# Optimization experiments

Measured on AMD Instinct MI355X. Metric: run time of the kernel, lower is better.

The kernel has to match this reference:

```python
import jax, jax.numpy as jnp
import numpy as np

B, IN_CH, HID, OUT_CH, GH, GW = 16, 64, 128, 64, 64, 64


def grid_edges(h, w):
    # torch_geometric.utils.grid: 8-neighborhood + self-loop, edge = (node, node+offset)
    idx = np.arange(h * w).reshape(h, w)
    rows, cols = [], []
    for dr in (-1, 0, 1):
        for dc in (-1, 0, 1):
            node = idx[max(0, -dr):h - max(0, dr), max(0, -dc):w - max(0, dc)]
            nb = idx[max(0, dr):h + min(0, dr) or None, max(0, dc):w + min(0, dc) or None]
            rows.append(node.ravel())
            cols.append(nb.ravel())
    return np.stack([np.concatenate(rows), np.concatenate(cols)])


def setup_inputs() -> dict:
    key = jax.random.key(0)
    ks = jax.random.split(key, 32)
    def rn(i, shape, scale=0.05):
        return jax.random.normal(ks[i], shape, dtype=jnp.float32) * scale
    e = grid_edges(GH, GW)                                   # (2, E)
    offs = (np.arange(B) * (GH * GW)).reshape(B, 1, 1)
    ei = (e[None] + offs).transpose(1, 0, 2).reshape(2, -1)  # (2, B*E) batched offsets
    return {
        "x": rn(0, (B, IN_CH, GH, GW), 1.0),
        "cW1": rn(1, (HID, IN_CH, 3, 3)), "cb1": rn(2, (HID,)),
        "cW2": rn(3, (IN_CH, HID, 3, 3)), "cb2": rn(4, (IN_CH,)),
        "q1W": rn(5, (HID, IN_CH)), "q1b": rn(6, (HID,)),
        "k1W": rn(7, (HID, IN_CH)), "k1b": rn(8, (HID,)),
        "v1W": rn(9, (HID, IN_CH)), "v1b": rn(10, (HID,)),
        "s1W": rn(11, (HID, IN_CH)), "s1b": rn(12, (HID,)),
        "q2W": rn(13, (IN_CH, HID)), "q2b": rn(14, (IN_CH,)),
        "k2W": rn(15, (IN_CH, HID)), "k2b": rn(16, (IN_CH,)),
        "v2W": rn(17, (IN_CH, HID)), "v2b": rn(18, (IN_CH,)),
        "s2W": rn(19, (IN_CH, HID)), "s2b": rn(20, (IN_CH,)),
        "fW1": rn(21, (HID, 2 * IN_CH, 3, 3)), "fb1": rn(22, (HID,)),
        "fW2": rn(23, (OUT_CH, HID, 3, 3)), "fb2": rn(24, (OUT_CH,)),
        "edge_index": jnp.asarray(ei, dtype=jnp.int32),
    }


def gelu(x):
    return jax.nn.gelu(x, approximate=False)


def sn_conv(x, W, b):
    # spectral_norm: power iteration on (O, I*k*k) matrix; u,v detached, grad through sigma
    O = W.shape[0]
    Wm = W.reshape(O, -1)
    u = jnp.ones((O,), W.dtype) / jnp.sqrt(jnp.asarray(O, W.dtype))
    for _ in range(3):
        v = Wm.T @ u
        v = v / (jnp.linalg.norm(v) + 1e-12)
        u = Wm @ v
        u = u / (jnp.linalg.norm(u) + 1e-12)
    u = jax.lax.stop_gradient(u)
    v = jax.lax.stop_gradient(v)
    sigma = u @ (Wm @ v)
    Wn = W / sigma
    xp = jnp.pad(x, ((0, 0), (0, 0), (1, 1), (1, 1)), mode='edge')  # replicate padding
    y = jax.lax.conv_general_dilated(xp, Wn, (1, 1), 'VALID',
                                     dimension_numbers=('NCHW', 'OIHW', 'NCHW'))
    return y + b[None, :, None, None]


def tconv(x, src, dst, N, heads, qW, qb, kW, kb, vW, vb, sW, sb):
    # PyG TransformerConv (concat=True, root_weight=True, no edge features)
    d = qW.shape[0] // heads
    q = (x @ qW.T + qb)[dst].reshape(-1, heads, d)
    k = (x @ kW.T + kb)[src].reshape(-1, heads, d)
    v = (x @ vW.T + vb)[src].reshape(-1, heads, d)
    alpha = (q * k).sum(-1) / jnp.sqrt(jnp.asarray(d, x.dtype))      # (E, heads)
    m = jax.ops.segment_max(alpha, dst, num_segments=N)               # scatter-softmax
    a = jnp.exp(alpha - m[dst])
    s = jax.ops.segment_sum(a, dst, num_segments=N)
    a = a / (s[dst] + 1e-16)
    out = jax.ops.segment_sum(a[:, :, None] * v, dst, num_segments=N)  # (N, heads, d)
    return out.reshape(N, heads * d) + x @ sW.T + sb


def reference(x, cW1, cb1, cW2, cb2, q1W, q1b, k1W, k1b, v1W, v1b, s1W, s1b,
              q2W, q2b, k2W, k2b, v2W, v2b, s2W, s2b, fW1, fb1, fW2, fb2, edge_index):
    Bb, C, Hc, Wc = x.shape
    N = Bb * Hc * Wc
    # CNN branch (DoubleConvBlock)
    x1 = gelu(sn_conv(gelu(sn_conv(x, cW1, cb1)), cW2, cb2))
    # GCN branch
    xf = x.transpose(0, 2, 3, 1).reshape(N, C)
    src, dst = edge_index[0], edge_index[1]
    h = gelu(tconv(xf, src, dst, N, 8, q1W, q1b, k1W, k1b, v1W, v1b, s1W, s1b))
    h = gelu(tconv(h, src, dst, N, 1, q2W, q2b, k2W, k2b, v2W, v2b, s2W, s2b))
    x2 = h.reshape(Bb, Hc, Wc, -1).transpose(0, 3, 1, 2)
    # Fusion
    xc = jnp.concatenate([x1, x2], axis=1)
    return gelu(sn_conv(gelu(sn_conv(xc, fW1, fb1)), fW2, fb2))
```

## Files before the change

### kernel.cpp

```cpp
#include <hip/hip_runtime.h>
#include <hip/hip_bf16.h>

typedef unsigned int  u32;
typedef unsigned short u16;
typedef __attribute__((ext_vector_type(8))) short bf16x8;
typedef __attribute__((ext_vector_type(4))) float f32x4;
typedef __attribute__((ext_vector_type(4))) u32 u32x4;

#define NPIX 65536

constexpr size_t SIG   = 0;
constexpr size_t B1OFF = 256;
constexpr size_t B2OFF = B1OFF + 2048;
constexpr size_t WC1   = B2OFF + 1024;
constexpr size_t WC2   = WC1 + 147456;
constexpr size_t WF1   = WC2 + 147456;
constexpr size_t WF2   = WF1 + 294912;
constexpr size_t WP1   = WF2 + 147456;
constexpr size_t WP2   = WP1 + 65536;
constexpr size_t XB    = WP2 + 65536;
constexpr size_t HBUF  = XB + 8388608;
constexpr size_t QKVS2 = HBUF + 16777216;
constexpr size_t XC    = QKVS2 + 33554432;
constexpr size_t QKVS1 = XC + 16777216;
constexpr size_t TBUF  = QKVS1 + 16777216;
constexpr size_t GRAM  = QKVS1 + 67108864;

__device__ __forceinline__ float gelu_f(float v) {
    float xa = fabsf(v) * 0.70710678118654752f;
    float t  = __fdividef(1.0f, fmaf(0.3275911f, xa, 1.0f));
    float poly = t * fmaf(t, fmaf(t, fmaf(t, fmaf(t, 1.061405429f, -1.453152027f),
                   1.421413741f), -0.284496736f), 0.254829592f);
    float erfv = 1.0f - poly * __expf(-xa * xa);
    erfv = copysignf(erfv, v);
    return 0.5f * v * (1.0f + erfv);
}
__device__ __forceinline__ u16 f2bf(float f) {
    __hip_bfloat16 b = __float2bfloat16(f);
    return *reinterpret_cast<u16*>(&b);
}
__device__ __forceinline__ float blo(u32 u) {
    union { u32 i; float f; } x; x.i = u << 16; return x.f;
}
__device__ __forceinline__ float bhi(u32 u) {
    union { u32 i; float f; } x; x.i = u & 0xffff0000u; return x.f;
}
__device__ __forceinline__ u32 packbf(float a, float b) {
    return (u32)f2bf(a) | ((u32)f2bf(b) << 16);
}
__device__ __forceinline__ void g2l16(const void* g, void* l) {
    __builtin_amdgcn_global_load_lds(
        (const __attribute__((address_space(1))) u32*)g,
        (__attribute__((address_space(3))) u32*)l, 16, 0, 0);
}

__device__ float block_sum(float vv, float* red) {
    #pragma unroll
    for (int m = 1; m < 64; m <<= 1) vv += __shfl_xor(vv, m);
    int tid = threadIdx.x;
    __syncthreads();
    if ((tid & 63) == 0) red[tid >> 6] = vv;
    __syncthreads();
    return red[0] + red[1] + red[2] + red[3];
}


__device__ void gram_body(int bid, char* smem,
                          const float* cW1, const float* cW2,
                          const float* fW1, const float* fW2, float* Gall) {
    const float* W; int O, K, wsel, tile;
    if (bid < 64)       { W = cW1; O = 128; K = 576;  wsel = 0; tile = bid; }
    else if (bid < 80)  { W = cW2; O = 64;  K = 1152; wsel = 1; tile = bid - 64; }
    else if (bid < 144) { W = fW1; O = 128; K = 1152; wsel = 2; tile = bid - 80; }
    else                { W = fW2; O = 64;  K = 1152; wsel = 3; tile = bid - 144; }
    int ntiles = O >> 4;
    int ti0 = (tile / ntiles) << 4, tj0 = (tile % ntiles) << 4;
    float (*Wi)[33] = (float(*)[33])smem;
    float (*Wj)[33] = (float(*)[33])(smem + 16 * 33 * 4);
    int tid = threadIdx.x;
    int ti = tid >> 4, tj = tid & 15;
    int r = tid >> 5, c = tid & 31;
    float acc = 0.f;
    for (int k0 = 0; k0 < K; k0 += 32) {
        Wi[r][c]     = W[(size_t)(ti0 + r) * K + k0 + c];
        Wi[r + 8][c] = W[(size_t)(ti0 + r + 8) * K + k0 + c];
        Wj[r][c]     = W[(size_t)(tj0 + r) * K + k0 + c];
        Wj[r + 8][c] = W[(size_t)(tj0 + r + 8) * K + k0 + c];
        __syncthreads();
        #pragma unroll
        for (int k = 0; k < 32; ++k)
            acc += Wi[ti][k] * Wj[tj][k];
        __syncthreads();
    }
    Gall[wsel * 16384 + (ti0 + ti) * 128 + (tj0 + tj)] = acc;
}

__device__ void convert_body(int bid, char* smem,
                             const float* __restrict__ x, u16* __restrict__ xb) {
    float (*tile)[65] = (float(*)[65])smem;
    int b = bid >> 6, y = bid & 63;
    int tid = threadIdx.x;
    #pragma unroll
    for (int i = 0; i < 16; ++i) {
        int c = (tid >> 6) + i * 4;
        tile[c][tid & 63] = x[(((size_t)b * 64 + c) << 12) + (y << 6) + (tid & 63)];
    }
    __syncthreads();
    #pragma unroll
    for (int i = 0; i < 16; ++i) {
        int idx = tid + i * 256;
        int p = idx >> 6, c = idx & 63;
        xb[(((size_t)b << 12) + (y << 6) + p) * 64 + c] = f2bf(tile[c][p]);
    }
}

__device__ void prep_proj_body(int bid,
               const float* q1W, const float* k1W, const float* v1W, const float* s1W,
               const float* q2W, const float* k2W, const float* v2W, const float* s2W,
               const float* q1b, const float* k1b, const float* v1b, const float* s1b,
               const float* q2b, const float* k2b, const float* v2b, const float* s2b,
               u16* wp1, u16* wp2, float* b1, float* b2) {
    const float* W1[4] = {q1W, k1W, v1W, s1W};
    const float* W2[4] = {q2W, k2W, v2W, s2W};
    const float* Bb1[4] = {q1b, k1b, v1b, s1b};
    const float* Bb2[4] = {q2b, k2b, v2b, s2b};
    int idx = bid * 256 + threadIdx.x;
    if (idx < 32768) {
        int w = idx >> 13, r = idx & 8191;
        wp1[(size_t)w * 8192 + r] = f2bf(W1[w][r]);
    } else if (idx < 65536) {
        int j = idx - 32768; int w = j >> 13, r = j & 8191;
        wp2[(size_t)w * 8192 + r] = f2bf(W2[w][r]);
    } else if (idx < 66048) {
        int j = idx - 65536; int w = j >> 7; b1[j] = Bb1[w][j & 127];
    } else if (idx < 66304) {
        int j = idx - 66048; int w = j >> 6; b2[j] = Bb2[w][j & 63];
    }
}

__device__ void prep_conv_w_body(int bx, int wsel,
                 const float* __restrict__ cW1, const float* __restrict__ cW2,
                 const float* __restrict__ fW1, const float* __restrict__ fW2,
                 const float* __restrict__ sig,
                 u16* wc1, u16* wc2, u16* wf1, u16* wf2) {
    const float* src; u16* dst; int O, C;
    switch (wsel) {
        case 0:  src = cW1; dst = wc1; O = 128; C = 64;  break;
        case 1:  src = cW2; dst = wc2; O = 64;  C = 128; break;
        case 2:  src = fW1; dst = wf1; O = 128; C = 128; break;
        default: src = fW2; dst = wf2; O = 64;  C = 128; break;
    }
    int idx = bx * 256 + threadIdx.x;
    if (idx >= O * C * 9) return;
    int o = idx / (C * 9);
    int rem = idx - o * (C * 9);
    int ci = rem / 9, tap = rem - ci * 9;
    float v = src[idx] / sig[wsel];
    dst[(size_t)o * (C * 9) + tap * C + ci] = f2bf(v);
}

template<int TAPS, int CC, int BN, int OUTM>
__device__ void mm_body(int bx, int by, char* smem,
               const u16* __restrict__ A, const u16* __restrict__ Bw,
               const float* __restrict__ bias, void* __restrict__ Cout,
               int ostride, int ocol0, int do_gelu) {
    constexpr int K = CC * TAPS;
    constexpr int NSTEP = TAPS;
    constexpr int NCH = CC / 8;
    constexpr int NKS = CC / 32;
    constexpr int NF = BN / 32;
    constexpr int HN = BN / 2;
    constexpr int RSTEP = 256 / NCH;
    constexpr int ALD = 128 / RSTEP;
    constexpr int BLD = BN / RSTEP;
    u16* Als = (u16*)smem;
    u16* Bls = (u16*)smem + 128 * CC;
    const int tid = threadIdx.x;
    const int w = tid >> 6;
    const int lane = tid & 63;
    const int m0 = bx * 128;
    const int nt0 = by * BN;
    const int wm = w >> 1, wn = w & 1;

    const int srow = tid / NCH;
    const int sslot = tid % NCH;
    const int csrc = ((sslot ^ (srow & (NCH - 1))) << 3);
    const u16* Bbase = Bw + (size_t)(nt0 + srow) * K + csrc;

    int offA[NKS][4], offB[NKS][NF];
    #pragma unroll
    for (int ks = 0; ks < NKS; ++ks) {
        #pragma unroll
        for (int mf = 0; mf < 4; ++mf) {
            int R = wm * 64 + mf * 16 + (lane & 15);
            int slot = (ks * 4 + (lane >> 4)) ^ (R & (NCH - 1));
            offA[ks][mf] = R * CC + slot * 8;
        }
        #pragma unroll
        for (int nf = 0; nf < NF; ++nf) {
            int Rb = wn * HN + nf * 16 + (lane & 15);
            int slot = (ks * 4 + (lane >> 4)) ^ (Rb & (NCH - 1));
            offB[ks][nf] = Rb * CC + slot * 8;
        }
    }

    f32x4 acc[4][NF];
    #pragma unroll
    for (int i = 0; i < 4; ++i)
        #pragma unroll
        for (int j = 0; j < NF; ++j) {
            f32x4 z = {0.f, 0.f, 0.f, 0.f};
            acc[i][j] = z;
        }

    #pragma unroll
    for (int kt = 0; kt < NSTEP; ++kt) {
        const int kk = kt * CC;
        const int dy = (TAPS == 9) ? (kt / 3 - 1) : 0;
        const int dx = (TAPS == 9) ? (kt % 3 - 1) : 0;
        #pragma unroll
        for (int i = 0; i < ALD; ++i) {
            const int m = m0 + srow + i * RSTEP;
            const u16* ga;
            if constexpr (TAPS == 9) {
                int yy = ((m >> 6) & 63) + dy; yy = min(max(yy, 0), 63);
                int xx = (m & 63) + dx;        xx = min(max(xx, 0), 63);
                ga = A + (size_t)((m & ~4095) | (yy << 6) | xx) * CC + csrc;
            } else {
                ga = A + (size_t)m * CC + csrc;
            }
            g2l16(ga, &Als[(srow + i * RSTEP) * CC + sslot * 8]);
        }
        #pragma unroll
        for (int i = 0; i < BLD; ++i)
            g2l16(Bbase + (size_t)i * RSTEP * K + kk,
                  &Bls[(srow + i * RSTEP) * CC + sslot * 8]);

        __syncthreads();

        #pragma unroll
        for (int ks = 0; ks < NKS; ++ks) {
            bf16x8 af[4];
            #pragma unroll
            for (int mf = 0; mf < 4; ++mf)
                af[mf] = *reinterpret_cast<const bf16x8*>(&Als[offA[ks][mf]]);
            #pragma unroll
            for (int nf = 0; nf < NF; ++nf) {
                bf16x8 bfv = *reinterpret_cast<const bf16x8*>(&Bls[offB[ks][nf]]);
                #pragma unroll
                for (int mf = 0; mf < 4; ++mf)
                    acc[mf][nf] = __builtin_amdgcn_mfma_f32_16x16x32_bf16(
                        af[mf], bfv, acc[mf][nf], 0, 0, 0);
            }
        }
        if (kt + 1 < NSTEP) __syncthreads();
    }

    #pragma unroll
    for (int mf = 0; mf < 4; ++mf) {
        int mrow = m0 + wm * 64 + mf * 16 + (lane >> 4) * 4;
        #pragma unroll
        for (int nf = 0; nf < NF; ++nf) {
            int col = nt0 + wn * HN + nf * 16 + (lane & 15);
            float bv = bias[col];
            if (OUTM == 0) {
                u16* Co = (u16*)Cout;
                #pragma unroll
                for (int j = 0; j < 4; ++j) {
                    float v = acc[mf][nf][j] + bv;
                    if (do_gelu) v = gelu_f(v);
                    Co[(size_t)(mrow + j) * ostride + ocol0 + col] = f2bf(v);
                }
            } else {
                float* Co = (float*)Cout;
                int b = m0 >> 12;
                int pixb = (mrow & 4095);
                f32x4 vv;
                #pragma unroll
                for (int j = 0; j < 4; ++j)
                    vv[j] = gelu_f(acc[mf][nf][j] + bv);
                *reinterpret_cast<f32x4*>(&Co[((size_t)(b * 64 + col)) * 4096 + pixb]) = vv;
            }
        }
    }
}

template<int CC, int BN, int NGRP>
__device__ void proj_body(int bx, char* smem,
               const u16* __restrict__ A, const u16* __restrict__ Bw,
               const float* __restrict__ bias, u16* __restrict__ Cout,
               int ostride) {
    constexpr int NCH = CC / 8;
    constexpr int NKS = CC / 32;
    constexpr int NF = BN / 32;
    constexpr int HN = BN / 2;
    constexpr int RSTEP = 256 / NCH;
    constexpr int ALD = 128 / RSTEP;
    constexpr int BLD = BN / RSTEP;
    u16* Als = (u16*)smem;
    u16* Bls = (u16*)smem + 128 * CC;
    const int tid = threadIdx.x;
    const int w = tid >> 6;
    const int lane = tid & 63;
    const int m0 = bx * 128;
    const int wm = w >> 1, wn = w & 1;

    const int srow = tid / NCH;
    const int sslot = tid % NCH;
    const int csrc = ((sslot ^ (srow & (NCH - 1))) << 3);

    #pragma unroll
    for (int i = 0; i < ALD; ++i) {
        const int m = m0 + srow + i * RSTEP;
        g2l16(A + (size_t)m * CC + csrc,
              &Als[(srow + i * RSTEP) * CC + sslot * 8]);
    }

    int offA[NKS][4], offB[NKS][NF];
    #pragma unroll
    for (int ks = 0; ks < NKS; ++ks) {
        #pragma unroll
        for (int mf = 0; mf < 4; ++mf) {
            int R = wm * 64 + mf * 16 + (lane & 15);
            int slot = (ks * 4 + (lane >> 4)) ^ (R & (NCH - 1));
            offA[ks][mf] = R * CC + slot * 8;
        }
        #pragma unroll
        for (int nf = 0; nf < NF; ++nf) {
            int Rb = wn * HN + nf * 16 + (lane & 15);
            int slot = (ks * 4 + (lane >> 4)) ^ (Rb & (NCH - 1));
            offB[ks][nf] = Rb * CC + slot * 8;
        }
    }

    #pragma unroll
    for (int g = 0; g < NGRP; ++g) {
        const u16* Bbase = Bw + (size_t)(g * BN + srow) * CC + csrc;
        #pragma unroll
        for (int i = 0; i < BLD; ++i)
            g2l16(Bbase + (size_t)i * RSTEP * CC,
                  &Bls[(srow + i * RSTEP) * CC + sslot * 8]);
        __syncthreads();

        f32x4 acc[4][NF];
        #pragma unroll
        for (int i = 0; i < 4; ++i)
            #pragma unroll
            for (int j = 0; j < NF; ++j) {
                f32x4 z = {0.f, 0.f, 0.f, 0.f};
                acc[i][j] = z;
            }
        #pragma unroll
        for (int ks = 0; ks < NKS; ++ks) {
            bf16x8 af[4];
            #pragma unroll
            for (int mf = 0; mf < 4; ++mf)
                af[mf] = *reinterpret_cast<const bf16x8*>(&Als[offA[ks][mf]]);
            #pragma unroll
            for (int nf = 0; nf < NF; ++nf) {
                bf16x8 bfv = *reinterpret_cast<const bf16x8*>(&Bls[offB[ks][nf]]);
                #pragma unroll
                for (int mf = 0; mf < 4; ++mf)
                    acc[mf][nf] = __builtin_amdgcn_mfma_f32_16x16x32_bf16(
                        af[mf], bfv, acc[mf][nf], 0, 0, 0);
            }
        }
        #pragma unroll
        for (int mf = 0; mf < 4; ++mf) {
            int mrow = m0 + wm * 64 + mf * 16 + (lane >> 4) * 4;
            #pragma unroll
            for (int nf = 0; nf < NF; ++nf) {
                int col = g * BN + wn * HN + nf * 16 + (lane & 15);
                float bv = bias[col];
                #pragma unroll
                for (int j = 0; j < 4; ++j)
                    Cout[(size_t)(mrow + j) * ostride + col] =
                        f2bf(acc[mf][nf][j] + bv);
            }
        }
        if (g + 1 < NGRP) __syncthreads();
    }
}

__device__ void attn1_body(int bid, char* smem, const u16* __restrict__ qkvs,
                           u16* __restrict__ h) {
    u16* KV = (u16*)smem;
    const int tid = threadIdx.x;
    const int w = tid >> 6;
    const int lane = tid & 63;
    const int n0 = bid * 16;
    const int imgb = n0 & ~4095;
    const int y = (n0 >> 6) & 63;
    const int x0 = n0 & 63;

    for (int t = w; t < 27; t += 4) {
        const int r = 4 * t + (lane >> 4);
        const int isV = r >= 54;
        const int rr = isV ? r - 54 : r;
        const int ry = rr / 18, rx = rr - ry * 18;
        const int yy = min(max(y + ry - 1, 0), 63);
        const int xx = min(max(x0 - 1 + rx, 0), 63);
        const u16* g = qkvs + (size_t)(imgb + (yy << 6) + xx) * 512
                        + (isV ? 256 : 128) + (lane & 15) * 8;
        g2l16(g, KV + t * 512);
    }
    __syncthreads();

    const int l16 = tid & 15;
    const int nn = tid >> 4;
    const int n = n0 + nn;
    const int x = x0 + nn;
    const u32* qk = (const u32*)qkvs;
    const int nbase = (n << 8) + l16 * 4;
    const u32* Kl = (const u32*)KV;

    u32x4 qp = *(const u32x4*)(qk + nbase);
    float q[8];
    #pragma unroll
    for (int i = 0; i < 4; ++i) { q[2*i] = blo(qp[i]); q[2*i+1] = bhi(qp[i]); }

    float al[9];
    float mx = -1e30f;
    #pragma unroll
    for (int e = 0; e < 9; ++e) {
        const int dy = e / 3 - 1, dx = e % 3 - 1;
        const bool valid = (unsigned)(y + dy) < 64u && (unsigned)(x + dx) < 64u;
        const int rk = (dy + 1) * 18 + nn + dx + 1;
        u32x4 kp = *(const u32x4*)(Kl + rk * 64 + l16 * 4);
        float p = 0.f;
        #pragma unroll
        for (int i = 0; i < 4; ++i) {
            p = fmaf(q[2*i],   blo(kp[i]), p);
            p = fmaf(q[2*i+1], bhi(kp[i]), p);
        }
        p += __shfl_xor(p, 1);
        al[e] = valid ? p * 0.25f : -1e30f;
        mx = fmaxf(mx, al[e]);
    }
    float s = 0.f;
    #pragma unroll
    for (int e = 0; e < 9; ++e) { al[e] = __expf(al[e] - mx); s += al[e]; }

    float o[8] = {0.f, 0.f, 0.f, 0.f, 0.f, 0.f, 0.f, 0.f};
    #pragma unroll
    for (int e = 0; e < 9; ++e) {
        const int dy = e / 3 - 1, dx = e % 3 - 1;
        const int rk = (dy + 1) * 18 + nn + dx + 1;
        u32x4 vp = *(const u32x4*)(Kl + (54 + rk) * 64 + l16 * 4);
        const float a = al[e];
        #pragma unroll
        for (int i = 0; i < 4; ++i) {
            o[2*i]   = fmaf(a, blo(vp[i]), o[2*i]);
            o[2*i+1] = fmaf(a, bhi(vp[i]), o[2*i+1]);
        }
    }
    const float r = __fdividef(1.0f, s + 1e-16f);
    u32x4 sp = *(const u32x4*)(qk + nbase + 192);
    u32x4 res;
    #pragma unroll
    for (int i = 0; i < 4; ++i) {
        float h0 = gelu_f(fmaf(o[2*i],   r, blo(sp[i])));
        float h1 = gelu_f(fmaf(o[2*i+1], r, bhi(sp[i])));
        res[i] = packbf(h0, h1);
    }
    *(u32x4*)((u32*)h + (n << 6) + l16 * 4) = res;
}


__global__ __launch_bounds__(256)
void power_kernel(const float* __restrict__ Gall, float* __restrict__ sig) {
    int wsel = blockIdx.x;
    const float* G = Gall + wsel * 16384;
    const int O = (wsel == 0 || wsel == 2) ? 128 : 64;
    __shared__ float u[128], t[128], red[4];
    int tid = threadIdx.x;
    if (tid < O) u[tid] = 1.0f / sqrtf((float)O);
    __syncthreads();
    for (int it = 0; it < 3; ++it) {
        if (tid < O) {
            float s = 0.f;
            const float4* gr = reinterpret_cast<const float4*>(G + (size_t)tid * 128);
            for (int j = 0; j < O / 4; ++j) {
                float4 g = gr[j];
                s += g.x * u[4*j] + g.y * u[4*j+1] + g.z * u[4*j+2] + g.w * u[4*j+3];
            }
            t[tid] = s;
        }
        __syncthreads();
        float loc = (tid < O) ? t[tid] * t[tid] : 0.f;
        float nt = sqrtf(block_sum(loc, red));
        if (it == 2) {
            float locd = (tid < O) ? u[tid] * t[tid] : 0.f;
            float dot = block_sum(locd, red);
            if (tid == 0) sig[wsel] = nt / sqrtf(dot + 1e-24f);
        } else {
            if (tid < O) u[tid] = t[tid] / (nt + 1e-12f);
            __syncthreads();
        }
    }
}

__global__ __launch_bounds__(256)
void attn2_kernel(const u16* __restrict__ qkvs, u16* __restrict__ xc) {
    const int tid = threadIdx.x;
    const int l8 = tid & 7;
    const int n = blockIdx.x * 32 + (tid >> 3);
    const int y = (n >> 6) & 63, x = n & 63;
    const u32* qk = (const u32*)qkvs;
    const int nbase = (n << 7) + l8 * 4;

    u32x4 qp = *(const u32x4*)(qk + nbase);
    float q[8];
    #pragma unroll
    for (int i = 0; i < 4; ++i) { q[2*i] = blo(qp[i]); q[2*i+1] = bhi(qp[i]); }

    float al[9];
    float mx = -1e30f;
    #pragma unroll
    for (int e = 0; e < 9; ++e) {
        const int dy = e / 3 - 1, dx = e % 3 - 1;
        const bool valid = (unsigned)(y + dy) < 64u && (unsigned)(x + dx) < 64u;
        const int off = valid ? ((dy * 64 + dx) << 7) : 0;
        u32x4 kp = *(const u32x4*)(qk + nbase + off + 32);
        float p = 0.f;
        #pragma unroll
        for (int i = 0; i < 4; ++i) {
            p = fmaf(q[2*i],   blo(kp[i]), p);
            p = fmaf(q[2*i+1], bhi(kp[i]), p);
        }
        p += __shfl_xor(p, 1);
        p += __shfl_xor(p, 2);
        p += __shfl_xor(p, 4);
        al[e] = valid ? p * 0.125f : -1e30f;
        mx = fmaxf(mx, al[e]);
    }
    float s = 0.f;
    #pragma unroll
    for (int e = 0; e < 9; ++e) { al[e] = __expf(al[e] - mx); s += al[e]; }

    float o[8] = {0.f, 0.f, 0.f, 0.f, 0.f, 0.f, 0.f, 0.f};
    #pragma unroll
    for (int e = 0; e < 9; ++e) {
        const int dy = e / 3 - 1, dx = e % 3 - 1;
        const bool valid = (unsigned)(y + dy) < 64u && (unsigned)(x + dx) < 64u;
        const int off = valid ? ((dy * 64 + dx) << 7) : 0;
        u32x4 vp = *(const u32x4*)(qk + nbase + off + 64);
        const float a = al[e];
        #pragma unroll
        for (int i = 0; i < 4; ++i) {
            o[2*i]   = fmaf(a, blo(vp[i]), o[2*i]);
            o[2*i+1] = fmaf(a, bhi(vp[i]), o[2*i+1]);
        }
    }
    const float r = __fdividef(1.0f, s + 1e-16f);
    u32x4 sp = *(const u32x4*)(qk + nbase + 96);
    u32x4 res;
    #pragma unroll
    for (int i = 0; i < 4; ++i) {
        float h0 = gelu_f(fmaf(o[2*i],   r, blo(sp[i])));
        float h1 = gelu_f(fmaf(o[2*i+1], r, bhi(sp[i])));
        res[i] = packbf(h0, h1);
    }
    *(u32x4*)((u32*)xc + (n << 6) + 32 + l8 * 4) = res;
}

template<int TAPS, int CC, int BN, int OUTM>
__global__ __launch_bounds__(256)
void mm_kernel(const u16* __restrict__ A, const u16* __restrict__ Bw,
               const float* __restrict__ bias, void* __restrict__ Cout,
               int ostride, int ocol0, int do_gelu) {
    __shared__ __align__(16) char smem[(128 * CC + BN * CC) * 2];
    mm_body<TAPS, CC, BN, OUTM>(blockIdx.x, blockIdx.y, smem, A, Bw, bias, Cout,
                                ostride, ocol0, do_gelu);
}

__global__ __launch_bounds__(256)
void fuse_misc(const float* cW1, const float* cW2, const float* fW1,
               const float* fW2, float* Gall,
               const float* x, u16* xb,
               const float* q1W, const float* k1W, const float* v1W, const float* s1W,
               const float* q2W, const float* k2W, const float* v2W, const float* s2W,
               const float* q1b, const float* k1b, const float* v1b, const float* s1b,
               const float* q2b, const float* k2b, const float* v2b, const float* s2b,
               u16* wp1, u16* wp2, float* b1, float* b2) {
    __shared__ __align__(16) char smem[16640];
    int bid = blockIdx.x;
    if (bid < 1024)       convert_body(bid, smem, x, xb);
    else if (bid < 1184)  gram_body(bid - 1024, smem, cW1, cW2, fW1, fW2, Gall);
    else                  prep_proj_body(bid - 1184, q1W, k1W, v1W, s1W,
                                         q2W, k2W, v2W, s2W, q1b, k1b, v1b, s1b,
                                         q2b, k2b, v2b, s2b, wp1, wp2, b1, b2);
}

__global__ __launch_bounds__(256)
void fuse_p1_w(const u16* xb, const u16* wp1, const float* b1, u16* qkvs1,
               const float* cW1, const float* cW2, const float* fW1,
               const float* fW2, const float* sig,
               u16* wc1, u16* wc2, u16* wf1, u16* wf2) {
    __shared__ __align__(16) char smem[(128 * 64 + 128 * 64) * 2];
    int bid = blockIdx.x;
    if (bid < 512)
        proj_body<64, 128, 4>(bid, smem, xb, wp1, b1, qkvs1, 512);
    else {
        int wk = bid - 512;
        prep_conv_w_body(wk % 576, wk / 576, cW1, cW2, fW1, fW2, sig,
                         wc1, wc2, wf1, wf2);
    }
}

__global__ __launch_bounds__(256)
void fuse_c1_a1(const u16* xb, const u16* wc1, const float* cb1, u16* y1,
                const u16* qkvs1, u16* hbuf) {
    __shared__ __align__(16) char smem[(128 * 64 + 128 * 64) * 2];
    int bid = blockIdx.x;
    if (bid < 512)
        mm_body<9, 64, 128, 0>(bid, 0, smem, xb, wc1, cb1, (void*)y1, 128, 0, 1);
    else
        attn1_body(bid - 512, smem, qkvs1, hbuf);
}

__global__ __launch_bounds__(256)
void fuse_c2_p2(const u16* y1, const u16* wc2, const float* cb2, u16* xc,
                const u16* hbuf, const u16* wp2, const float* b2, u16* qkvs2) {
    __shared__ __align__(16) char smem[(128 * 128 + 128 * 128) * 2];
    int bid = blockIdx.x;
    if (bid < 512)
        mm_body<9, 128, 64, 0>(bid, 0, smem, y1, wc2, cb2, (void*)xc, 128, 0, 1);
    else
        proj_body<128, 128, 2>(bid - 512, smem, hbuf, wp2, b2, qkvs2, 256);
}

extern "C" void kernel_launch(void* const* d_in, const int* in_sizes, int n_in,
                              void* d_out, int out_size, void* d_ws, size_t ws_size,
                              hipStream_t stream) {
    const float* x   = (const float*)d_in[0];
    const float* cW1 = (const float*)d_in[1];
    const float* cb1 = (const float*)d_in[2];
    const float* cW2 = (const float*)d_in[3];
    const float* cb2 = (const float*)d_in[4];
    const float* q1W = (const float*)d_in[5];
    const float* q1b = (const float*)d_in[6];
    const float* k1W = (const float*)d_in[7];
    const float* k1b = (const float*)d_in[8];
    const float* v1W = (const float*)d_in[9];
    const float* v1b = (const float*)d_in[10];
    const float* s1W = (const float*)d_in[11];
    const float* s1b = (const float*)d_in[12];
    const float* q2W = (const float*)d_in[13];
    const float* q2b = (const float*)d_in[14];
    const float* k2W = (const float*)d_in[15];
    const float* k2b = (const float*)d_in[16];
    const float* v2W = (const float*)d_in[17];
    const float* v2b = (const float*)d_in[18];
    const float* s2W = (const float*)d_in[19];
    const float* s2b = (const float*)d_in[20];
    const float* fW1 = (const float*)d_in[21];
    const float* fb1 = (const float*)d_in[22];
    const float* fW2 = (const float*)d_in[23];
    const float* fb2 = (const float*)d_in[24];

    char* ws = (char*)d_ws;
    float* sig  = (float*)(ws + SIG);
    float* b1   = (float*)(ws + B1OFF);
    float* b2   = (float*)(ws + B2OFF);
    u16* wc1    = (u16*)(ws + WC1);
    u16* wc2    = (u16*)(ws + WC2);
    u16* wf1    = (u16*)(ws + WF1);
    u16* wf2    = (u16*)(ws + WF2);
    u16* wp1    = (u16*)(ws + WP1);
    u16* wp2    = (u16*)(ws + WP2);
    u16* xb     = (u16*)(ws + XB);
    u16* hbuf   = (u16*)(ws + HBUF);
    u16* qkvs2  = (u16*)(ws + QKVS2);
    u16* xc     = (u16*)(ws + XC);
    u16* qkvs1  = (u16*)(ws + QKVS1);
    u16* tbuf   = (u16*)(ws + TBUF);
    float* gram = (float*)(ws + GRAM);
    float* out  = (float*)d_out;
    u16* y1     = (u16*)d_out;

    fuse_misc<<<1444, 256, 0, stream>>>(cW1, cW2, fW1, fW2, gram, x, xb,
        q1W, k1W, v1W, s1W, q2W, k2W, v2W, s2W,
        q1b, k1b, v1b, s1b, q2b, k2b, v2b, s2b, wp1, wp2, b1, b2);
    power_kernel<<<4, 256, 0, stream>>>(gram, sig);
    fuse_p1_w<<<2816, 256, 0, stream>>>(xb, wp1, b1, qkvs1,
        cW1, cW2, fW1, fW2, sig, wc1, wc2, wf1, wf2);
    fuse_c1_a1<<<4608, 256, 0, stream>>>(xb, wc1, cb1, y1, qkvs1, hbuf);
    fuse_c2_p2<<<1024, 256, 0, stream>>>(y1, wc2, cb2, xc, hbuf, wp2, b2, qkvs2);
    attn2_kernel<<<NPIX / 32, 256, 0, stream>>>(qkvs2, xc);
    mm_kernel<9, 128, 128, 0><<<dim3(512, 1), 256, 0, stream>>>(
        xc, wf1, fb1, tbuf, 128, 0, 1);
    mm_kernel<9, 128, 64, 1><<<dim3(512, 1), 256, 0, stream>>>(
        tbuf, wf2, fb2, out, 0, 0, 1);
}
```

Baseline: 189.0 us.

## Load halo row strip once per kernel row and reuse across horizontal taps

Each conv block now stages two padded image rows (with left/right halo) for one vertical offset into shared memory. All three horizontal taps read from that strip with shifted row indices, instead of regathering the full 128-pixel A tile for each of the 9 taps. This cuts global/L2 gather traffic for the activation operand by about 3x. The cost is a different swizzle and indexing scheme, and larger shared memory for CC=128 (the 68-wide rows), which may affect occupancy in the standalone conv kernels.

```diff
diff --git a/kernel.cpp b/kernel.cpp
--- a/kernel.cpp
+++ b/kernel.cpp
@@ -159,50 +159,48 @@
     dst[(size_t)o * (C * 9) + tap * C + ci] = f2bf(v);
 }
 
-template<int TAPS, int CC, int BN, int OUTM>
-__device__ void mm_body(int bx, int by, char* smem,
+template<int CC, int BN, int OUTM>
+__device__ void conv_body(int bx, char* smem,
                const u16* __restrict__ A, const u16* __restrict__ Bw,
                const float* __restrict__ bias, void* __restrict__ Cout,
                int ostride, int ocol0, int do_gelu) {
-    constexpr int K = CC * TAPS;
-    constexpr int NSTEP = TAPS;
+    constexpr int K = CC * 9;
     constexpr int NCH = CC / 8;
     constexpr int NKS = CC / 32;
     constexpr int NF = BN / 32;
     constexpr int HN = BN / 2;
+    constexpr int CPL = 512 / CC;
+    constexpr int W = (CC == 64) ? 72 : 68;
+    constexpr int NLR = W / CPL;
     constexpr int RSTEP = 256 / NCH;
-    constexpr int ALD = 128 / RSTEP;
     constexpr int BLD = BN / RSTEP;
-    u16* Als = (u16*)smem;
-    u16* Bls = (u16*)smem + 128 * CC;
+    u16* Ah  = (u16*)smem;
+    u16* Bls = (u16*)smem + 2 * W * CC;
+
     const int tid = threadIdx.x;
     const int w = tid >> 6;
     const int lane = tid & 63;
+    const int wm = w >> 1, wn = w & 1;
     const int m0 = bx * 128;
-    const int nt0 = by * BN;
-    const int wm = w >> 1, wn = w & 1;
-
-    const int srow = tid / NCH;
-    const int sslot = tid % NCH;
-    const int csrc = ((sslot ^ (srow & (NCH - 1))) << 3);
-    const u16* Bbase = Bw + (size_t)(nt0 + srow) * K + csrc;
-
-    int offA[NKS][4], offB[NKS][NF];
-    #pragma unroll
-    for (int ks = 0; ks < NKS; ++ks) {
-        #pragma unroll
-        for (int mf = 0; mf < 4; ++mf) {
-            int R = wm * 64 + mf * 16 + (lane & 15);
-            int slot = (ks * 4 + (lane >> 4)) ^ (R & (NCH - 1));
-            offA[ks][mf] = R * CC + slot * 8;
-        }
+    const int img = m0 >> 12;
+    const int y0 = (m0 >> 6) & 63;
+    const int lr = lane & 15, lg = lane >> 4;
+
+    const int srowB = tid / NCH;
+    const int sslotB = tid % NCH;
+    const int csrcB = ((sslotB ^ (srowB & (NCH - 1))) << 3);
+    const int apos = lane / NCH;
+    const int achk = lane % NCH;
+
+    int offB[NKS][NF];
+    #pragma unroll
+    for (int ks = 0; ks < NKS; ++ks)
         #pragma unroll
         for (int nf = 0; nf < NF; ++nf) {
-            int Rb = wn * HN + nf * 16 + (lane & 15);
-            int slot = (ks * 4 + (lane >> 4)) ^ (Rb & (NCH - 1));
+            int Rb = wn * HN + nf * 16 + lr;
+            int slot = (ks * 4 + lg) ^ (Rb & (NCH - 1));
             offB[ks][nf] = Rb * CC + slot * 8;
         }
-    }
 
     f32x4 acc[4][NF];
     #pragma unroll
@@ -214,54 +212,58 @@
         }
 
     #pragma unroll
-    for (int kt = 0; kt < NSTEP; ++kt) {
-        const int kk = kt * CC;
-        const int dy = (TAPS == 9) ? (kt / 3 - 1) : 0;
-        const int dx = (TAPS == 9) ? (kt % 3 - 1) : 0;
-        #pragma unroll
-        for (int i = 0; i < ALD; ++i) {
-            const int m = m0 + srow + i * RSTEP;
-            const u16* ga;
-            if constexpr (TAPS == 9) {
-                int yy = ((m >> 6) & 63) + dy; yy = min(max(yy, 0), 63);
-                int xx = (m & 63) + dx;        xx = min(max(xx, 0), 63);
-                ga = A + (size_t)((m & ~4095) | (yy << 6) | xx) * CC + csrc;
-            } else {
-                ga = A + (size_t)m * CC + csrc;
+    for (int d = 0; d < 3; ++d) {
+        for (int t0 = 0; t0 < 2 * NLR; t0 += 4) {
+            int t = t0 + w;
+            if (t < 2 * NLR) {
+                int imgrow = t / NLR;
+                int pos0 = (t - imgrow * NLR) * CPL;
+                int yy = min(max(y0 + imgrow + d - 1, 0), 63);
+                int pos = pos0 + apos;
+                int xx = min(max(pos - 1, 0), 63);
+                int key = (imgrow * W + pos) & (NCH - 1);
+                const u16* g = A + (size_t)((img << 12) + (yy << 6) + xx) * CC
+                                 + ((achk ^ key) << 3);
+                g2l16(g, Ah + (size_t)(imgrow * W + pos0) * CC);
             }
-            g2l16(ga, &Als[(srow + i * RSTEP) * CC + sslot * 8]);
-        }
-        #pragma unroll
-        for (int i = 0; i < BLD; ++i)
-            g2l16(Bbase + (size_t)i * RSTEP * K + kk,
-                  &Bls[(srow + i * RSTEP) * CC + sslot * 8]);
-
-        __syncthreads();
-
-        #pragma unroll
-        for (int ks = 0; ks < NKS; ++ks) {
-            bf16x8 af[4];
+        }
+        #pragma unroll
+        for (int dxi = 0; dxi < 3; ++dxi) {
+            const int tap = d * 3 + dxi;
             #pragma unroll
-            for (int mf = 0; mf < 4; ++mf)
-                af[mf] = *reinterpret_cast<const bf16x8*>(&Als[offA[ks][mf]]);
+            for (int i = 0; i < BLD; ++i)
+                g2l16(Bw + (size_t)(srowB + i * RSTEP) * K + tap * CC + csrcB,
+                      Bls + (size_t)(srowB + i * RSTEP) * CC + sslotB * 8);
+            __syncthreads();
+
             #pragma unroll
-            for (int nf = 0; nf < NF; ++nf) {
-                bf16x8 bfv = *reinterpret_cast<const bf16x8*>(&Bls[offB[ks][nf]]);
+            for (int ks = 0; ks < NKS; ++ks) {
+                bf16x8 af[4];
                 #pragma unroll
-                for (int mf = 0; mf < 4; ++mf)
-                    acc[mf][nf] = __builtin_amdgcn_mfma_f32_16x16x32_bf16(
-                        af[mf], bfv, acc[mf][nf], 0, 0, 0);
+                for (int mf = 0; mf < 4; ++mf) {
+                    int r = wm * W + mf * 16 + lr + dxi;
+                    int addr = r * CC + (((ks * 4 + lg) ^ (r & (NCH - 1))) << 3);
+                    af[mf] = *reinterpret_cast<const bf16x8*>(&Ah[addr]);
+                }
+                #pragma unroll
+                for (int nf = 0; nf < NF; ++nf) {
+                    bf16x8 bfv = *reinterpret_cast<const bf16x8*>(&Bls[offB[ks][nf]]);
+                    #pragma unroll
+                    for (int mf = 0; mf < 4; ++mf)
+                        acc[mf][nf] = __builtin_amdgcn_mfma_f32_16x16x32_bf16(
+                            af[mf], bfv, acc[mf][nf], 0, 0, 0);
+                }
             }
-        }
-        if (kt + 1 < NSTEP) __syncthreads();
+            if (tap < 8) __syncthreads();
+        }
     }
 
     #pragma unroll
     for (int mf = 0; mf < 4; ++mf) {
-        int mrow = m0 + wm * 64 + mf * 16 + (lane >> 4) * 4;
+        int mrow = m0 + wm * 64 + mf * 16 + lg * 4;
         #pragma unroll
         for (int nf = 0; nf < NF; ++nf) {
-            int col = nt0 + wn * HN + nf * 16 + (lane & 15);
+            int col = wn * HN + nf * 16 + lr;
             float bv = bias[col];
             if (OUTM == 0) {
                 u16* Co = (u16*)Cout;
@@ -564,14 +566,15 @@
     *(u32x4*)((u32*)xc + (n << 6) + 32 + l8 * 4) = res;
 }
 
-template<int TAPS, int CC, int BN, int OUTM>
+template<int CC, int BN, int OUTM>
 __global__ __launch_bounds__(256)
-void mm_kernel(const u16* __restrict__ A, const u16* __restrict__ Bw,
-               const float* __restrict__ bias, void* __restrict__ Cout,
-               int ostride, int ocol0, int do_gelu) {
-    __shared__ __align__(16) char smem[(128 * CC + BN * CC) * 2];
-    mm_body<TAPS, CC, BN, OUTM>(blockIdx.x, blockIdx.y, smem, A, Bw, bias, Cout,
-                                ostride, ocol0, do_gelu);
+void conv_kernel(const u16* __restrict__ A, const u16* __restrict__ Bw,
+                 const float* __restrict__ bias, void* __restrict__ Cout,
+                 int ostride, int ocol0, int do_gelu) {
+    constexpr int W = (CC == 64) ? 72 : 68;
+    __shared__ __align__(16) char smem[(2 * W * CC + BN * CC) * 2];
+    conv_body<CC, BN, OUTM>(blockIdx.x, smem, A, Bw, bias, Cout,
+                            ostride, ocol0, do_gelu);
 }
 
 __global__ __launch_bounds__(256)
@@ -611,10 +614,10 @@
 __global__ __launch_bounds__(256)
 void fuse_c1_a1(const u16* xb, const u16* wc1, const float* cb1, u16* y1,
                 const u16* qkvs1, u16* hbuf) {
-    __shared__ __align__(16) char smem[(128 * 64 + 128 * 64) * 2];
+    __shared__ __align__(16) char smem[(2 * 72 * 64 + 128 * 64) * 2];
     int bid = blockIdx.x;
     if (bid < 512)
-        mm_body<9, 64, 128, 0>(bid, 0, smem, xb, wc1, cb1, (void*)y1, 128, 0, 1);
+        conv_body<64, 128, 0>(bid, smem, xb, wc1, cb1, (void*)y1, 128, 0, 1);
     else
         attn1_body(bid - 512, smem, qkvs1, hbuf);
 }
@@ -625,7 +628,7 @@
     __shared__ __align__(16) char smem[(128 * 128 + 128 * 128) * 2];
     int bid = blockIdx.x;
     if (bid < 512)
-        mm_body<9, 128, 64, 0>(bid, 0, smem, y1, wc2, cb2, (void*)xc, 128, 0, 1);
+        conv_body<128, 64, 0>(bid, smem, y1, wc2, cb2, (void*)xc, 128, 0, 1);
     else
         proj_body<128, 128, 2>(bid - 512, smem, hbuf, wp2, b2, qkvs2, 256);
 }
@@ -688,8 +691,8 @@
     fuse_c1_a1<<<4608, 256, 0, stream>>>(xb, wc1, cb1, y1, qkvs1, hbuf);
     fuse_c2_p2<<<1024, 256, 0, stream>>>(y1, wc2, cb2, xc, hbuf, wp2, b2, qkvs2);
     attn2_kernel<<<NPIX / 32, 256, 0, stream>>>(qkvs2, xc);
-    mm_kernel<9, 128, 128, 0><<<dim3(512, 1), 256, 0, stream>>>(
+    conv_kernel<128, 128, 0><<<512, 256, 0, stream>>>(
         xc, wf1, fb1, tbuf, 128, 0, 1);
-    mm_kernel<9, 128, 64, 1><<<dim3(512, 1), 256, 0, stream>>>(
+    conv_kernel<128, 64, 1><<<512, 256, 0, stream>>>(
         tbuf, wf2, fb2, out, 0, 0, 1);
 }
```

Measured after the change: 188.5 us. No clear change (-0.3%).
